# Performance work log

Measured on AMD Instinct MI355X. Metric: run time of the kernel, lower is better.

Reference implementation:

```python
import jax, jax.numpy as jnp
import numpy as np

B, S, I, H, O = 64, 512, 1024, 1024, 1024


def setup_inputs() -> dict:
    key = jax.random.key(0)
    ks = jax.random.split(key, 10)
    s = 0.02
    return {
        "x": jax.random.normal(ks[0], (B, S, I), dtype=jnp.float32),
        "W_hi": jax.random.normal(ks[1], (H, H), dtype=jnp.float32) * s,
        "W_ii": jax.random.normal(ks[2], (I, H), dtype=jnp.float32) * s,
        "W_hf": jax.random.normal(ks[3], (H, H), dtype=jnp.float32) * s,
        "W_if": jax.random.normal(ks[4], (I, H), dtype=jnp.float32) * s,
        "W_ho": jax.random.normal(ks[5], (H, H), dtype=jnp.float32) * s,
        "W_io": jax.random.normal(ks[6], (I, H), dtype=jnp.float32) * s,
        "W_hg": jax.random.normal(ks[7], (H, H), dtype=jnp.float32) * s,
        "W_ig": jax.random.normal(ks[8], (I, H), dtype=jnp.float32) * s,
        "W_y": jax.random.normal(ks[9], (H, O), dtype=jnp.float32) * s,
    }


def reference(x, W_hi, W_ii, W_hf, W_if, W_ho, W_io, W_hg, W_ig, W_y):
    b = x.shape[0]
    h0 = jnp.zeros((b, W_hi.shape[0]), dtype=x.dtype)
    c0 = jnp.zeros_like(h0)

    def step(carry, x_t):
        h, c = carry
        i = jax.nn.sigmoid(h @ W_hi + x_t @ W_ii)
        f = jax.nn.sigmoid(h @ W_hf + x_t @ W_if)
        o = jax.nn.sigmoid(h @ W_ho + x_t @ W_io)
        g = jnp.tanh(h @ W_hg + x_t @ W_ig)
        c = f * c + i * g
        h = o * jnp.tanh(c)
        return (h, c), None

    # scan over time: x -> [S, B, I]
    (h_T, _), _ = jax.lax.scan(step, (h0, c0), jnp.swapaxes(x, 0, 1))
    return h_T @ W_y
```

## Files before the change

### kernel.cpp

```cpp
#include <hip/hip_runtime.h>


typedef __bf16 bfv8 __attribute__((ext_vector_type(8)));
typedef float f32x4 __attribute__((ext_vector_type(4)));
typedef unsigned int u32v4 __attribute__((ext_vector_type(4)));

__device__ __forceinline__ unsigned short f2bf(float x) {
    union { float f; unsigned int u; } v; v.f = x;
    unsigned int r = (v.u + 0x7FFFu + ((v.u >> 16) & 1u)) >> 16;
    return (unsigned short)r;
}
__device__ __forceinline__ float bf2f(unsigned short s) {
    union { unsigned int u; float f; } v; v.u = ((unsigned int)s) << 16;
    return v.f;
}

struct SrcPtrs { const float* p[9]; };

#define ISSUE8(A, P, O0, O1, O2, O3, O4, O5, O6, O7)                         \
    asm volatile(                                                            \
        "global_load_dwordx4 %0, %8, off offset:" O0 " sc0 sc1\n\t"          \
        "global_load_dwordx4 %1, %8, off offset:" O1 " sc0 sc1\n\t"          \
        "global_load_dwordx4 %2, %8, off offset:" O2 " sc0 sc1\n\t"          \
        "global_load_dwordx4 %3, %8, off offset:" O3 " sc0 sc1\n\t"          \
        "global_load_dwordx4 %4, %8, off offset:" O4 " sc0 sc1\n\t"          \
        "global_load_dwordx4 %5, %8, off offset:" O5 " sc0 sc1\n\t"          \
        "global_load_dwordx4 %6, %8, off offset:" O6 " sc0 sc1\n\t"          \
        "global_load_dwordx4 %7, %8, off offset:" O7 " sc0 sc1"              \
        : "=&v"(A[0]), "=&v"(A[1]), "=&v"(A[2]), "=&v"(A[3]),                \
          "=&v"(A[4]), "=&v"(A[5]), "=&v"(A[6]), "=&v"(A[7])                 \
        : "v"(P)                                                             \
        : "memory")

#define WAIT8(N, A)                                                          \
    do {                                                                     \
        asm volatile("s_waitcnt vmcnt(" N ")"                                \
                     : "+v"(A[0]), "+v"(A[1]), "+v"(A[2]), "+v"(A[3]),       \
                       "+v"(A[4]), "+v"(A[5]), "+v"(A[6]), "+v"(A[7])        \
                     :: "memory");                                           \
        __builtin_amdgcn_sched_barrier(0);                                   \
    } while (0)

#define CONSUME8(A, IT0)                                                     \
    _Pragma("unroll")                                                        \
    for (int j = 0; j < 8; ++j) {                                            \
        _Pragma("unroll")                                                    \
        for (int n = 0; n < 2; ++n) {                                        \
            const int off = (((((IT0) + j) << 1) | n) << 10) + (lane << 4);  \
            acc[n] = __builtin_amdgcn_mfma_f32_16x16x32_bf16(                \
                A[j], *(const bfv8*)(Lw + off), acc[n], 0, 0, 0);            \
        }                                                                    \
    }

__global__ __launch_bounds__(256) void pack_weights(SrcPtrs sp,
                                                    unsigned short* __restrict__ Whp,
                                                    unsigned short* __restrict__ Wip,
                                                    unsigned short* __restrict__ Wy) {
    __shared__ float tile[64][65];
    const int z = blockIdx.z;
    const float* __restrict__ src = sp.p[z];
    const int n0 = blockIdx.x * 64, k0 = blockIdx.y * 64;
    const int tc = threadIdx.x & 63, tq = threadIdx.x >> 6;

    #pragma unroll
    for (int r = 0; r < 16; ++r) {
        const int kk = tq * 16 + r;
        tile[kk][tc] = src[(size_t)(k0 + kk) * 1024 + n0 + tc];
    }
    __syncthreads();
    #pragma unroll
    for (int r = 0; r < 16; ++r) {
        const int nl = tq * 16 + r;
        const int n = n0 + nl;
        const int k = k0 + tc;
        const unsigned short v = f2bf(tile[tc][nl]);
        if (z < 8) {
            const int g = z & 3;
            const int blk = n >> 3;
            const int c = (g << 3) | (n & 7);
            const int lanef = (c & 15) | (((k >> 3) & 3) << 4);
            const size_t off = ((size_t)((((blk << 5) | (k >> 5)) << 1) | (c >> 4)) << 9)
                             + (lanef << 3) + (k & 7);
            (z < 4 ? Whp : Wip)[off] = v;
        } else {
            Wy[(size_t)n * 1024 + k] = v;
        }
    }
}

__global__ __launch_bounds__(256) void convert_x(const float* __restrict__ x,
                                                 unsigned short* __restrict__ xT) {
    const size_t gid = (size_t)blockIdx.x * 256 + threadIdx.x;
    const int i0 = (int)(gid & 255) * 4;
    const size_t row = gid >> 8;
    const int t = (int)(row >> 6), b = (int)(row & 63);
    const float4 v = *reinterpret_cast<const float4*>(x + (((size_t)b * 512 + t) << 10) + i0);
    ushort4 o;
    o.x = f2bf(v.x); o.y = f2bf(v.y); o.z = f2bf(v.z); o.w = f2bf(v.w);
    *reinterpret_cast<ushort4*>(xT + (row << 10) + i0) = o;
}

__global__ __launch_bounds__(256) void lstm_pc(const unsigned short* __restrict__ xT,
                                               const unsigned short* __restrict__ Whp,
                                               const unsigned short* __restrict__ Wip,
                                               unsigned short* __restrict__ h0,
                                               unsigned short* __restrict__ h1,
                                               int* __restrict__ flg,
                                               int* __restrict__ xflg,
                                               unsigned short* __restrict__ ring) {
    __shared__ struct {
        __align__(16) unsigned char wp[65536];
        __align__(16) unsigned char pad[32768];
        __align__(16) unsigned short hs[64][8];
        int sig;
        int Lrdy[4];
    } L;
    unsigned char* Lw = L.wp;

    const int tid = threadIdx.x;
    const int w = tid >> 6;
    const int lane = tid & 63;
    const int lr = lane & 15;
    const int kq = lane >> 4;
    const bool isFactory = (blockIdx.x >= 128);
    const int b = isFactory ? (blockIdx.x - 128) : blockIdx.x;

    {
        const unsigned short* src = (isFactory ? Wip : Whp) + ((size_t)b << 15);
        #pragma unroll
        for (int s = 0; s < 16; ++s) {
            const int c = s * 256 + tid;
            *(bfv8*)(L.wp + c * 16) = *(const bfv8*)(src + c * 8);
        }
    }
    if (tid == 0) L.sig = 0;
    if (tid < 4) L.Lrdy[tid] = 0;
    __syncthreads();

    if (isFactory) {
        for (int tt = 0; tt < 512; ++tt) {
            if (tt >= 8) {
                const int* cf = flg + (b << 9);
                while (__hip_atomic_load(cf, __ATOMIC_RELAXED, __HIP_MEMORY_SCOPE_AGENT) < tt - 7)
                    __builtin_amdgcn_s_sleep(2);
            }
            const unsigned short* __restrict__ Ax =
                xT + ((size_t)tt << 16) + (size_t)((w << 4) + lr) * 1024 + kq * 8;
            f32x4 xacc[2] = {};
            #pragma unroll 8
            for (int it = 0; it < 32; ++it) {
                const bfv8 a = *reinterpret_cast<const bfv8*>(Ax + it * 32);
                #pragma unroll
                for (int n = 0; n < 2; ++n) {
                    const int off = (((it << 1) | n) << 10) + (lane << 4);
                    xacc[n] = __builtin_amdgcn_mfma_f32_16x16x32_bf16(
                        a, *(const bfv8*)(Lw + off), xacc[n], 0, 0, 0);
                }
            }
            unsigned short vv[8];
            #pragma unroll
            for (int n = 0; n < 2; ++n)
                #pragma unroll
                for (int r = 0; r < 4; ++r)
                    vv[n * 4 + r] = f2bf(xacc[n][r]);
            unsigned short* rp = ring + (((size_t)(b << 3) + (tt & 7)) * 4 + w) * 512 + lane * 8;
            asm volatile("global_store_dwordx4 %0, %1, off sc0 sc1"
                         :: "v"(rp), "v"(*(const u32v4*)vv) : "memory");
            asm volatile("s_waitcnt vmcnt(0)" ::: "memory");
            if (lane == 0) {
                const int old = atomicAdd(&L.sig, 1);
                if (old == 4 * tt + 3)
                    asm volatile("global_store_dword %0, %1, off sc0 sc1"
                                 :: "v"(xflg + (b << 9)), "v"(tt + 1) : "memory");
            }
        }
        return;
    }

    float cst[4] = {0.f, 0.f, 0.f, 0.f};
    const int mw = w;
    const int hoff = ((mw << 4) + lr) * 1024 + kq * 8;

    for (int t = 0; t < 512; ++t) {
        const unsigned short* __restrict__ hin  = (t & 1) ? h1 : h0;
        unsigned short* __restrict__       hout = (t & 1) ? h0 : h1;

        const int* xfp = xflg + (b << 9);
        while (__hip_atomic_load(xfp, __ATOMIC_RELAXED, __HIP_MEMORY_SCOPE_AGENT) < t + 1)
            __builtin_amdgcn_s_sleep(1);
        u32v4 xp;
        {
            const unsigned short* rp =
                ring + (((size_t)(b << 3) + (t & 7)) * 4 + mw) * 512 + lane * 8;
            asm volatile("global_load_dwordx4 %0, %1, off sc0 sc1"
                         : "=v"(xp) : "v"(rp) : "memory");
        }

        if (t > 0) {
            const int* fp = flg + (((mw << 5) + (lane & 31)) << 9);
            for (;;) {
                const int f = __hip_atomic_load(fp, __ATOMIC_RELAXED,
                                                __HIP_MEMORY_SCOPE_AGENT);
                if (__all(f >= t)) break;
                __builtin_amdgcn_s_sleep(1);
            }
            __hip_atomic_store(&L.Lrdy[mw], t, __ATOMIC_RELAXED,
                               __HIP_MEMORY_SCOPE_WORKGROUP);
        }
        auto ldswait = [&](int g) {
            if (t == 0) return;
            while (__hip_atomic_load(&L.Lrdy[g], __ATOMIC_RELAXED,
                                     __HIP_MEMORY_SCOPE_WORKGROUP) < t) { }
            asm volatile("" ::: "memory");
        };

        const unsigned short* hp = hin + hoff;
        f32x4 acc[2] = {};
        bfv8 a0[8], a1[8];
        ldswait(0);
        ISSUE8(a0, hp, "0", "64", "128", "192", "256", "320", "384", "448");
        ldswait(1);
        ISSUE8(a1, hp, "512", "576", "640", "704", "768", "832", "896", "960");
        WAIT8("8", a0);
        CONSUME8(a0, 0);
        ldswait(2);
        ISSUE8(a0, hp, "1024", "1088", "1152", "1216", "1280", "1344", "1408", "1472");
        WAIT8("8", a1);
        CONSUME8(a1, 8);
        ldswait(3);
        ISSUE8(a1, hp, "1536", "1600", "1664", "1728", "1792", "1856", "1920", "1984");
        WAIT8("8", a0);
        CONSUME8(a0, 16);
        WAIT8("0", a1);
        CONSUME8(a1, 24);

        asm volatile("s_waitcnt vmcnt(0)" : "+v"(xp) :: "memory");
        __builtin_amdgcn_sched_barrier(0);
        {
            const unsigned short* xs = (const unsigned short*)&xp;
            #pragma unroll
            for (int n = 0; n < 2; ++n)
                #pragma unroll
                for (int r = 0; r < 4; ++r)
                    acc[n][r] += bf2f(xs[n * 4 + r]);
        }

        const bool low = (lr & 8) == 0;
        unsigned short hsv[4];
        #pragma unroll
        for (int r = 0; r < 4; ++r) {
            const float s0 = acc[0][r], s1 = acc[1][r];
            const float x0 = __shfl_xor(s0, 8);
            const float x1 = __shfl_xor(s1, 8);
            const float pi = low ? s0 : x0;
            const float pf = low ? x0 : s0;
            const float po = low ? s1 : x1;
            const float pg = low ? x1 : s1;
            const float ig = 1.f / (1.f + __expf(-pi));
            const float fg = 1.f / (1.f + __expf(-pf));
            const float og = 1.f / (1.f + __expf(-po));
            const float gg = 1.f - 2.f / (__expf(2.f * pg) + 1.f);
            const float cn = fg * cst[r] + ig * gg;
            cst[r] = cn;
            hsv[r] = f2bf(og * (1.f - 2.f / (__expf(2.f * cn) + 1.f)));
        }

        if (low) {
            #pragma unroll
            for (int r = 0; r < 4; ++r)
                L.hs[(mw << 4) + (kq << 2) + r][lr] = hsv[r];
        }
        asm volatile("s_waitcnt lgkmcnt(0)" ::: "memory");
        __builtin_amdgcn_sched_barrier(0);
        if (lane < 16) {
            const int row = (mw << 4) + lane;
            const u32v4 hv = *reinterpret_cast<const u32v4*>(&L.hs[row][0]);
            asm volatile("global_store_dwordx4 %0, %1, off sc0 sc1"
                         :: "v"(hout + (size_t)row * 1024 + (b << 3)), "v"(hv)
                         : "memory");
        }
        asm volatile("s_waitcnt vmcnt(0)" ::: "memory");
        if (lane == 0) {
            const int old = atomicAdd(&L.sig, 1);
            if (old == 4 * t + 3)
                asm volatile("global_store_dword %0, %1, off sc0 sc1"
                             :: "v"(flg + (b << 9)), "v"(t + 1) : "memory");
        }
    }
}

__global__ __launch_bounds__(512) void lstm_fb(const unsigned short* __restrict__ xT,
                                               const unsigned short* __restrict__ Whp,
                                               const unsigned short* __restrict__ Wip,
                                               unsigned short* __restrict__ h0,
                                               unsigned short* __restrict__ h1,
                                               int* __restrict__ flg) {
    __shared__ struct {
        __align__(16) unsigned char wh[65536];
        __align__(16) unsigned char wi[65536];
        float xb[2][2][4][256];
        __align__(16) unsigned short hs[64][8];
        int sig;
    } L;
    unsigned char* Lw = L.wh;

    const int tid = threadIdx.x;
    const int w = tid >> 6;
    const int lane = tid & 63;
    const int lr = lane & 15;
    const int kq = lane >> 4;
    const int blk = blockIdx.x;
    const int mw = w & 3;
    const bool isX = (w >= 4);

    #pragma unroll
    for (int s = 0; s < 8; ++s) {
        const int c = s * 512 + tid;
        *(bfv8*)(L.wh + c * 16) = *(const bfv8*)(Whp + ((size_t)blk << 15) + c * 8);
        *(bfv8*)(L.wi + c * 16) = *(const bfv8*)(Wip + ((size_t)blk << 15) + c * 8);
    }
    if (tid == 0) L.sig = 0;
    __syncthreads();

    auto xwork = [&](int tt) {
        const unsigned short* __restrict__ Ax =
            xT + ((size_t)tt << 16) + (size_t)((mw << 4) + lr) * 1024 + kq * 8;
        f32x4 xacc[2] = {};
        #pragma unroll 8
        for (int it = 0; it < 32; ++it) {
            const bfv8 a = *reinterpret_cast<const bfv8*>(Ax + it * 32);
            #pragma unroll
            for (int n = 0; n < 2; ++n) {
                const int off = (((it << 1) | n) << 10) + (lane << 4);
                xacc[n] = __builtin_amdgcn_mfma_f32_16x16x32_bf16(
                    a, *(const bfv8*)(L.wi + off), xacc[n], 0, 0, 0);
            }
        }
        #pragma unroll
        for (int n = 0; n < 2; ++n)
            #pragma unroll
            for (int r = 0; r < 4; ++r)
                L.xb[tt & 1][n][r][(mw << 6) + lane] = xacc[n][r];
    };

    if (isX) xwork(0);
    __syncthreads();

    float cst[4] = {0.f, 0.f, 0.f, 0.f};
    const int hoff = ((mw << 4) + lr) * 1024 + kq * 8;

    for (int t = 0; t < 512; ++t) {
        const unsigned short* __restrict__ hin  = (t & 1) ? h1 : h0;
        unsigned short* __restrict__       hout = (t & 1) ? h0 : h1;

        if (!isX) {
            auto poll32 = [&](int g) {
                if (t == 0) return;
                const int* fp = flg + (((g << 5) + (lane & 31)) << 9);
                for (;;) {
                    const int f = __hip_atomic_load(fp, __ATOMIC_RELAXED,
                                                    __HIP_MEMORY_SCOPE_AGENT);
                    if (__all(f >= t)) break;
                    __builtin_amdgcn_s_sleep(1);
                }
            };
            const unsigned short* hp = hin + hoff;
            f32x4 acc[2] = {};
            bfv8 a0[8], a1[8];
            poll32(0);
            ISSUE8(a0, hp, "0", "64", "128", "192", "256", "320", "384", "448");
            poll32(1);
            ISSUE8(a1, hp, "512", "576", "640", "704", "768", "832", "896", "960");
            WAIT8("8", a0);
            CONSUME8(a0, 0);
            poll32(2);
            ISSUE8(a0, hp, "1024", "1088", "1152", "1216", "1280", "1344", "1408", "1472");
            WAIT8("8", a1);
            CONSUME8(a1, 8);
            poll32(3);
            ISSUE8(a1, hp, "1536", "1600", "1664", "1728", "1792", "1856", "1920", "1984");
            WAIT8("8", a0);
            CONSUME8(a0, 16);
            WAIT8("0", a1);
            CONSUME8(a1, 24);

            #pragma unroll
            for (int n = 0; n < 2; ++n)
                #pragma unroll
                for (int r = 0; r < 4; ++r)
                    acc[n][r] += L.xb[t & 1][n][r][(mw << 6) + lane];

            const bool low = (lr & 8) == 0;
            unsigned short hsv[4];
            #pragma unroll
            for (int r = 0; r < 4; ++r) {
                const float s0 = acc[0][r], s1 = acc[1][r];
                const float x0 = __shfl_xor(s0, 8);
                const float x1 = __shfl_xor(s1, 8);
                const float pi = low ? s0 : x0;
                const float pf = low ? x0 : s0;
                const float po = low ? s1 : x1;
                const float pg = low ? x1 : s1;
                const float ig = 1.f / (1.f + __expf(-pi));
                const float fg = 1.f / (1.f + __expf(-pf));
                const float og = 1.f / (1.f + __expf(-po));
                const float gg = 1.f - 2.f / (__expf(2.f * pg) + 1.f);
                const float cn = fg * cst[r] + ig * gg;
                cst[r] = cn;
                hsv[r] = f2bf(og * (1.f - 2.f / (__expf(2.f * cn) + 1.f)));
            }
            if (low) {
                #pragma unroll
                for (int r = 0; r < 4; ++r)
                    L.hs[(mw << 4) + (kq << 2) + r][lr] = hsv[r];
            }
            asm volatile("s_waitcnt lgkmcnt(0)" ::: "memory");
            __builtin_amdgcn_sched_barrier(0);
            if (lane < 16) {
                const int row = (mw << 4) + lane;
                const u32v4 hv = *reinterpret_cast<const u32v4*>(&L.hs[row][0]);
                asm volatile("global_store_dwordx4 %0, %1, off sc0 sc1"
                             :: "v"(hout + (size_t)row * 1024 + (blk << 3)), "v"(hv)
                             : "memory");
            }
            asm volatile("s_waitcnt vmcnt(0)" ::: "memory");
            if (lane == 0) {
                const int old = atomicAdd(&L.sig, 1);
                if (old == 4 * t + 3)
                    asm volatile("global_store_dword %0, %1, off sc0 sc1"
                                 :: "v"(flg + (blk << 9)), "v"(t + 1) : "memory");
            }
        } else {
            if (t + 1 < 512) xwork(t + 1);
        }
        __syncthreads();
    }
}

__global__ __launch_bounds__(256) void final_gemm(const unsigned short* __restrict__ h_in,
                                                  const unsigned short* __restrict__ WyT,
                                                  float* __restrict__ out) {
    const int tid = threadIdx.x;
    const int w = tid >> 6;
    const int lane = tid & 63;
    const int lr = lane & 15;
    const int kq = lane >> 4;
    const int c0 = blockIdx.x * 16;
    const int k0 = w * 256;

    f32x4 acc[4] = {};
    #pragma unroll 2
    for (int it = 0; it < 8; ++it) {
        const int k = k0 + it * 32 + kq * 8;
        const bfv8 bfr = *reinterpret_cast<const bfv8*>(WyT + (size_t)(c0 + lr) * 1024 + k);
        #pragma unroll
        for (int m = 0; m < 4; ++m) {
            const bfv8 a = *reinterpret_cast<const bfv8*>(h_in + (size_t)(m * 16 + lr) * 1024 + k);
            acc[m] = __builtin_amdgcn_mfma_f32_16x16x32_bf16(a, bfr, acc[m], 0, 0, 0);
        }
    }
    __shared__ float red[4][64][17];
    #pragma unroll
    for (int m = 0; m < 4; ++m)
        #pragma unroll
        for (int r = 0; r < 4; ++r)
            red[w][m * 16 + kq * 4 + r][lr] = acc[m][r];
    __syncthreads();
    #pragma unroll
    for (int u = 0; u < 4; ++u) {
        const int item = u * 256 + tid;
        const int b = item >> 4;
        const int jr = item & 15;
        const float s = red[0][b][jr] + red[1][b][jr] + red[2][b][jr] + red[3][b][jr];
        out[b * 1024 + c0 + jr] = s;
    }
}

extern "C" void kernel_launch(void* const* d_in, const int* in_sizes, int n_in,
                              void* d_out, int out_size, void* d_ws, size_t ws_size,
                              hipStream_t stream) {
    const float* x = (const float*)d_in[0];
    SrcPtrs sp;
    sp.p[0] = (const float*)d_in[1];
    sp.p[1] = (const float*)d_in[3];
    sp.p[2] = (const float*)d_in[5];
    sp.p[3] = (const float*)d_in[7];
    sp.p[4] = (const float*)d_in[2];
    sp.p[5] = (const float*)d_in[4];
    sp.p[6] = (const float*)d_in[6];
    sp.p[7] = (const float*)d_in[8];
    sp.p[8] = (const float*)d_in[9];

    char* ws = (char*)d_ws;
    unsigned short* Whp  = (unsigned short*)(ws + 0);
    unsigned short* Wip  = (unsigned short*)(ws + 8388608);
    unsigned short* Wy   = (unsigned short*)(ws + 16777216);
    unsigned short* xT   = (unsigned short*)(ws + 18874368);
    unsigned short* h0   = (unsigned short*)(ws + 85983232);
    unsigned short* h1   = (unsigned short*)(ws + 86114304);
    int*            flg  = (int*)(ws + 86245376);
    int*            xflg = (int*)(ws + 86507520);
    unsigned short* ring = (unsigned short*)(ws + 86769664);

    const bool split = ws_size >= 90963968ull;

    pack_weights<<<dim3(16, 16, 9), 256, 0, stream>>>(sp, Whp, Wip, Wy);
    convert_x<<<32768, 256, 0, stream>>>(x, xT);
    hipMemsetAsync(h0, 0, 131072, stream);
    hipMemsetAsync(flg, 0, 262144, stream);

    if (split) {
        hipMemsetAsync(xflg, 0, 262144, stream);
        lstm_pc<<<256, 256, 0, stream>>>(xT, Whp, Wip, h0, h1, flg, xflg, ring);
    } else {
        lstm_fb<<<128, 512, 0, stream>>>(xT, Whp, Wip, h0, h1, flg);
    }

    final_gemm<<<64, 256, 0, stream>>>(h0, Wy, (float*)d_out);
}
```

Before: 3.492 ms.

## Fuse x fp32-to-bf16 conversion into factory blocks and use append-only h ring

Removes the separate convert_x pass: the factory blocks now read fp32 x directly and convert it to bf16 in registers before the MFMA input projection. The hidden state moves from ping-pong buffers to an append-only ring indexed by timestep, so each step's h has a unique address. That lets the h loads drop the sc0 sc1 coherence bits, and the h stores gain a nontemporal hint. The trade-off is double the x read bandwidth in the factory, and the new hring sizing and placement need to be checked against ws_size.

```diff
diff --git a/kernel.cpp b/kernel.cpp
--- a/kernel.cpp
+++ b/kernel.cpp
@@ -13,6 +13,13 @@
 __device__ __forceinline__ float bf2f(unsigned short s) {
     union { unsigned int u; float f; } v; v.u = ((unsigned int)s) << 16;
     return v.f;
+}
+__device__ __forceinline__ bfv8 cvt8(const float* p) {
+    const float4 f0 = *reinterpret_cast<const float4*>(p);
+    const float4 f1 = *reinterpret_cast<const float4*>(p + 4);
+    unsigned short u[8] = {f2bf(f0.x), f2bf(f0.y), f2bf(f0.z), f2bf(f0.w),
+                           f2bf(f1.x), f2bf(f1.y), f2bf(f1.z), f2bf(f1.w)};
+    return *reinterpret_cast<const bfv8*>(u);
 }
 
 struct SrcPtrs { const float* p[9]; };
@@ -27,6 +34,21 @@
         "global_load_dwordx4 %5, %8, off offset:" O5 " sc0 sc1\n\t"          \
         "global_load_dwordx4 %6, %8, off offset:" O6 " sc0 sc1\n\t"          \
         "global_load_dwordx4 %7, %8, off offset:" O7 " sc0 sc1"              \
+        : "=&v"(A[0]), "=&v"(A[1]), "=&v"(A[2]), "=&v"(A[3]),                \
+          "=&v"(A[4]), "=&v"(A[5]), "=&v"(A[6]), "=&v"(A[7])                 \
+        : "v"(P)                                                             \
+        : "memory")
+
+#define ISSUE8C(A, P, O0, O1, O2, O3, O4, O5, O6, O7)                        \
+    asm volatile(                                                            \
+        "global_load_dwordx4 %0, %8, off offset:" O0 "\n\t"                  \
+        "global_load_dwordx4 %1, %8, off offset:" O1 "\n\t"                  \
+        "global_load_dwordx4 %2, %8, off offset:" O2 "\n\t"                  \
+        "global_load_dwordx4 %3, %8, off offset:" O3 "\n\t"                  \
+        "global_load_dwordx4 %4, %8, off offset:" O4 "\n\t"                  \
+        "global_load_dwordx4 %5, %8, off offset:" O5 "\n\t"                  \
+        "global_load_dwordx4 %6, %8, off offset:" O6 "\n\t"                  \
+        "global_load_dwordx4 %7, %8, off offset:" O7                         \
         : "=&v"(A[0]), "=&v"(A[1]), "=&v"(A[2]), "=&v"(A[3]),                \
           "=&v"(A[4]), "=&v"(A[5]), "=&v"(A[6]), "=&v"(A[7])                 \
         : "v"(P)                                                             \
@@ -100,11 +122,10 @@
     *reinterpret_cast<ushort4*>(xT + (row << 10) + i0) = o;
 }
 
-__global__ __launch_bounds__(256) void lstm_pc(const unsigned short* __restrict__ xT,
+__global__ __launch_bounds__(256) void lstm_pc(const float* __restrict__ x,
                                                const unsigned short* __restrict__ Whp,
                                                const unsigned short* __restrict__ Wip,
-                                               unsigned short* __restrict__ h0,
-                                               unsigned short* __restrict__ h1,
+                                               unsigned short* __restrict__ hring,
                                                int* __restrict__ flg,
                                                int* __restrict__ xflg,
                                                unsigned short* __restrict__ ring) {
@@ -138,18 +159,19 @@
     __syncthreads();
 
     if (isFactory) {
+        const float* __restrict__ Axb =
+            x + (size_t)((w << 4) + lr) * 524288 + kq * 8;
         for (int tt = 0; tt < 512; ++tt) {
             if (tt >= 8) {
                 const int* cf = flg + (b << 9);
                 while (__hip_atomic_load(cf, __ATOMIC_RELAXED, __HIP_MEMORY_SCOPE_AGENT) < tt - 7)
                     __builtin_amdgcn_s_sleep(2);
             }
-            const unsigned short* __restrict__ Ax =
-                xT + ((size_t)tt << 16) + (size_t)((w << 4) + lr) * 1024 + kq * 8;
+            const float* __restrict__ Ax = Axb + (size_t)tt * 1024;
             f32x4 xacc[2] = {};
             #pragma unroll 8
             for (int it = 0; it < 32; ++it) {
-                const bfv8 a = *reinterpret_cast<const bfv8*>(Ax + it * 32);
+                const bfv8 a = cvt8(Ax + it * 32);
                 #pragma unroll
                 for (int n = 0; n < 2; ++n) {
                     const int off = (((it << 1) | n) << 10) + (lane << 4);
@@ -182,8 +204,8 @@
     const int hoff = ((mw << 4) + lr) * 1024 + kq * 8;
 
     for (int t = 0; t < 512; ++t) {
-        const unsigned short* __restrict__ hin  = (t & 1) ? h1 : h0;
-        unsigned short* __restrict__       hout = (t & 1) ? h0 : h1;
+        const unsigned short* __restrict__ hin  = hring + ((size_t)t << 16);
+        unsigned short* __restrict__       hout = hring + ((size_t)(t + 1) << 16);
 
         const int* xfp = xflg + (b << 9);
         while (__hip_atomic_load(xfp, __ATOMIC_RELAXED, __HIP_MEMORY_SCOPE_AGENT) < t + 1)
@@ -218,17 +240,17 @@
         f32x4 acc[2] = {};
         bfv8 a0[8], a1[8];
         ldswait(0);
-        ISSUE8(a0, hp, "0", "64", "128", "192", "256", "320", "384", "448");
+        ISSUE8C(a0, hp, "0", "64", "128", "192", "256", "320", "384", "448");
         ldswait(1);
-        ISSUE8(a1, hp, "512", "576", "640", "704", "768", "832", "896", "960");
+        ISSUE8C(a1, hp, "512", "576", "640", "704", "768", "832", "896", "960");
         WAIT8("8", a0);
         CONSUME8(a0, 0);
         ldswait(2);
-        ISSUE8(a0, hp, "1024", "1088", "1152", "1216", "1280", "1344", "1408", "1472");
+        ISSUE8C(a0, hp, "1024", "1088", "1152", "1216", "1280", "1344", "1408", "1472");
         WAIT8("8", a1);
         CONSUME8(a1, 8);
         ldswait(3);
-        ISSUE8(a1, hp, "1536", "1600", "1664", "1728", "1792", "1856", "1920", "1984");
+        ISSUE8C(a1, hp, "1536", "1600", "1664", "1728", "1792", "1856", "1920", "1984");
         WAIT8("8", a0);
         CONSUME8(a0, 16);
         WAIT8("0", a1);
@@ -275,7 +297,7 @@
         if (lane < 16) {
             const int row = (mw << 4) + lane;
             const u32v4 hv = *reinterpret_cast<const u32v4*>(&L.hs[row][0]);
-            asm volatile("global_store_dwordx4 %0, %1, off sc0 sc1"
+            asm volatile("global_store_dwordx4 %0, %1, off sc0 sc1 nt"
                          :: "v"(hout + (size_t)row * 1024 + (b << 3)), "v"(hv)
                          : "memory");
         }
@@ -492,29 +514,36 @@
     sp.p[8] = (const float*)d_in[9];
 
     char* ws = (char*)d_ws;
-    unsigned short* Whp  = (unsigned short*)(ws + 0);
-    unsigned short* Wip  = (unsigned short*)(ws + 8388608);
-    unsigned short* Wy   = (unsigned short*)(ws + 16777216);
-    unsigned short* xT   = (unsigned short*)(ws + 18874368);
-    unsigned short* h0   = (unsigned short*)(ws + 85983232);
-    unsigned short* h1   = (unsigned short*)(ws + 86114304);
-    int*            flg  = (int*)(ws + 86245376);
-    int*            xflg = (int*)(ws + 86507520);
-    unsigned short* ring = (unsigned short*)(ws + 86769664);
-
-    const bool split = ws_size >= 90963968ull;
+    unsigned short* Whp = (unsigned short*)(ws + 0);
+    unsigned short* Wip = (unsigned short*)(ws + 8388608);
+    unsigned short* Wy  = (unsigned short*)(ws + 16777216);
 
     pack_weights<<<dim3(16, 16, 9), 256, 0, stream>>>(sp, Whp, Wip, Wy);
-    convert_x<<<32768, 256, 0, stream>>>(x, xT);
-    hipMemsetAsync(h0, 0, 131072, stream);
-    hipMemsetAsync(flg, 0, 262144, stream);
-
+
+    const bool split = ws_size >= 90832896ull;
     if (split) {
+        int*            flg   = (int*)(ws + 18874368);
+        int*            xflg  = (int*)(ws + 19136512);
+        unsigned short* ring  = (unsigned short*)(ws + 19398656);
+        unsigned short* hring = (unsigned short*)(ws + 23592960);
+
+        hipMemsetAsync(hring, 0, 131072, stream);
+        hipMemsetAsync(flg, 0, 262144, stream);
         hipMemsetAsync(xflg, 0, 262144, stream);
-        lstm_pc<<<256, 256, 0, stream>>>(xT, Whp, Wip, h0, h1, flg, xflg, ring);
+
+        lstm_pc<<<256, 256, 0, stream>>>(x, Whp, Wip, hring, flg, xflg, ring);
+        final_gemm<<<64, 256, 0, stream>>>(hring + ((size_t)512 << 16), Wy, (float*)d_out);
     } else {
+        unsigned short* xT = (unsigned short*)(ws + 18874368);
+        unsigned short* h0 = (unsigned short*)(ws + 85983232);
+        unsigned short* h1 = (unsigned short*)(ws + 86114304);
+        int*            flg = (int*)(ws + 86245376);
+
+        convert_x<<<32768, 256, 0, stream>>>(x, xT);
+        hipMemsetAsync(h0, 0, 131072, stream);
+        hipMemsetAsync(flg, 0, 262144, stream);
+
         lstm_fb<<<128, 512, 0, stream>>>(xT, Whp, Wip, h0, h1, flg);
-    }
-
-    final_gemm<<<64, 256, 0, stream>>>(h0, Wy, (float*)d_out);
-}
+        final_gemm<<<64, 256, 0, stream>>>(h0, Wy, (float*)d_out);
+    }
+}
```

Result: slower. 4.263 ms (+22.1%).
